# Performance work log

Hardware: AMD Instinct MI355X
Metric: run time of the kernel (lower is better)

## Reference

```python
import jax, jax.numpy as jnp
import numpy as np

N_NODES = 20000
N_EDGES = 320000
C = 64  # classes
NEG_SLOPE = 0.2  # DGL GATConv default


def setup_inputs() -> dict:
    key = jax.random.key(0)
    ks = jax.random.split(key, 32)
    dims = [C, 2 * C, 4 * C, 8 * C, 16 * C]
    inp = {}
    inp["feat"] = jax.random.normal(ks[0], (N_NODES, C), jnp.float32)
    k = 1
    for i in range(4):
        din, dout = dims[i], dims[i + 1]
        scale = 1.0 / np.sqrt(din)
        inp[f"W{i+1}"] = jax.random.normal(ks[k], (din, dout), jnp.float32) * scale; k += 1
        inp[f"al{i+1}"] = jax.random.normal(ks[k], (dout,), jnp.float32) * 0.1; k += 1
        inp[f"ar{i+1}"] = jax.random.normal(ks[k], (dout,), jnp.float32) * 0.1; k += 1
        inp[f"b{i+1}"] = jnp.zeros((dout,), jnp.float32)
    inp["relW"] = jax.random.normal(ks[k], (16 * C, C), jnp.float32) * (1.0 / np.sqrt(16 * C)); k += 1
    inp["relB"] = jnp.zeros((C,), jnp.float32)
    inp["src"] = jax.random.randint(ks[k], (N_EDGES,), 0, N_NODES, jnp.int32); k += 1
    inp["dst"] = jax.random.randint(ks[k], (N_EDGES,), 0, N_NODES, jnp.int32); k += 1
    inp["rel"] = jnp.ones((C,), jnp.int32)
    inp["order"] = 1023
    return inp


def _gat_layer(x, W, al, ar, b, src, dst, n_nodes):
    """DGL GATConv (num_heads=1, allow_zero_in_degree=True, activation=tanh)."""
    h = x @ W                                   # [N, D] projected features
    el = h @ al                                 # [N] attn_l score per node
    er = h @ ar                                 # [N] attn_r score per node
    e = jax.nn.leaky_relu(el[src] + er[dst], NEG_SLOPE)          # [E]
    # segment (edge) softmax over incoming edges of each dst node
    m = jax.ops.segment_max(e, dst, num_segments=n_nodes)        # [N]
    ex = jnp.exp(e - m[dst])                                      # [E]
    s = jax.ops.segment_sum(ex, dst, num_segments=n_nodes)       # [N]
    alpha = ex / s[dst]                                           # [E]
    # gather neighbor messages, weight by attention, scatter-add to dst
    out = jax.ops.segment_sum(h[src] * alpha[:, None], dst, num_segments=n_nodes)  # [N, D]
    return jnp.tanh(out + b)


def reference(feat, W1, al1, ar1, b1, W2, al2, ar2, b2, W3, al3, ar3, b3,
              W4, al4, ar4, b4, relW, relB, src, dst, rel, order):
    n = feat.shape[0]
    h = _gat_layer(feat, W1, al1, ar1, b1, src, dst, n)
    h = _gat_layer(h, W2, al2, ar2, b2, src, dst, n)
    h = _gat_layer(h, W3, al3, ar3, b3, src, dst, n)
    h = _gat_layer(h, W4, al4, ar4, b4, src, dst, n)
    embeddings = h[: order + 1]                  # first order+1 node embeddings
    pooling = jnp.mean(embeddings, axis=0)       # [16C]
    logits = pooling @ relW + relB               # [C]
    nz = jnp.nonzero(rel, size=rel.shape[0])[0]  # static-size nonzero (rel is all-ones)
    return logits[nz]
```

## Files before the change

kernel.cpp:

```cpp
#include <hip/hip_runtime.h>
#include <hip/hip_bf16.h>

#define NN 20000
#define NE 320000
#define MPAD 20096
#define ORD 1024

typedef __hip_bfloat16 bf16;
typedef __attribute__((ext_vector_type(8))) short bf16x8;
typedef __attribute__((ext_vector_type(4))) float f32x4;

static __device__ __forceinline__ float b2f(bf16 x) { return __bfloat162float(x); }
static __device__ __forceinline__ float bfbits2f(short s) {
    unsigned int u = ((unsigned int)(unsigned short)s) << 16;
    float f; __builtin_memcpy(&f, &u, 4); return f;
}
static __device__ __forceinline__ short f2bfbits(float v) {
    bf16 h = __float2bfloat16(v);
    short s; __builtin_memcpy(&s, &h, 2); return s;
}
static __device__ __forceinline__ unsigned short f2bfu(float v) {
    bf16 h = __float2bfloat16(v);
    unsigned short s; __builtin_memcpy(&s, &h, 2); return s;
}

__global__ void setup_all(const float* __restrict__ feat,
                          const float* __restrict__ W1, const float* __restrict__ al1, const float* __restrict__ ar1,
                          const float* __restrict__ W2, const float* __restrict__ al2, const float* __restrict__ ar2,
                          const float* __restrict__ W3, const float* __restrict__ al3, const float* __restrict__ ar3,
                          const float* __restrict__ W4, const float* __restrict__ al4, const float* __restrict__ ar4,
                          bf16* __restrict__ featb, bf16* __restrict__ wt1,
                          bf16* __restrict__ wt2, bf16* __restrict__ wt3,
                          bf16* __restrict__ wt4, int* __restrict__ counts,
                          float* __restrict__ walbuf, float* __restrict__ warbuf) {
    int b = blockIdx.x;
    if (b < 960) {
        const float *W, *al, *ar; int dout, k; float *wal, *war;
        if (b < 64)       { W = W1; al = al1; ar = ar1; dout = 128;  k = b;       wal = walbuf;        war = warbuf; }
        else if (b < 192) { W = W2; al = al2; ar = ar2; dout = 256;  k = b - 64;  wal = walbuf + 512;  war = warbuf + 512; }
        else if (b < 448) { W = W3; al = al3; ar = ar3; dout = 512;  k = b - 192; wal = walbuf + 1024; war = warbuf + 1024; }
        else              { W = W4; al = al4; ar = ar4; dout = 1024; k = b - 448; wal = walbuf + 1536; war = warbuf + 1536; }
        const float* row = W + (long)k * dout;
        float sl = 0.f, sr = 0.f;
        for (int j = threadIdx.x; j < dout; j += 256) {
            float w = row[j];
            sl += w * al[j];
            sr += w * ar[j];
        }
        __shared__ float sbl[256], sbr[256];
        sbl[threadIdx.x] = sl; sbr[threadIdx.x] = sr;
        __syncthreads();
        for (int st = 128; st > 0; st >>= 1) {
            if (threadIdx.x < st) {
                sbl[threadIdx.x] += sbl[threadIdx.x + st];
                sbr[threadIdx.x] += sbr[threadIdx.x + st];
            }
            __syncthreads();
        }
        if (threadIdx.x == 0) { wal[k] = sbl[0]; war[k] = sbr[0]; }
        return;
    }
    int i = (b - 960) * 256 + threadIdx.x;
    if (i < NN) counts[i] = 0;
    if (i < 1280000) { featb[i] = __float2bfloat16(feat[i]); return; }
    i -= 1280000;
    if (i < 8192)  { int r = i >> 7,  c = i & 127;  wt1[c * 64 + r]  = __float2bfloat16(W1[i]); return; }
    i -= 8192;
    if (i < 32768) { int r = i >> 8,  c = i & 255;  wt2[c * 128 + r] = __float2bfloat16(W2[i]); return; }
    i -= 32768;
    if (i < 131072){ int r = i >> 9,  c = i & 511;  wt3[c * 256 + r] = __float2bfloat16(W3[i]); return; }
    i -= 131072;
    if (i < 524288){ int r = i >> 10, c = i & 1023; wt4[c * 512 + r] = __float2bfloat16(W4[i]); return; }
}

__global__ void hist_kernel(const int* __restrict__ dst, int* __restrict__ counts, int n) {
    int i = blockIdx.x * blockDim.x + threadIdx.x;
    if (i < n) atomicAdd(&counts[dst[i]], 1);
}

__global__ void scan_sort(const int* __restrict__ counts, int* __restrict__ offsets,
                          int* __restrict__ cursor, int* __restrict__ nodeperm, int n) {
    const int T = 1024;
    int tid = threadIdx.x;
    int per = (n + T - 1) / T;
    int base = tid * per;
    int local = 0;
    for (int i = 0; i < per; i++) {
        int idx = base + i;
        if (idx < n) local += counts[idx];
    }
    __shared__ int sums[T];
    sums[tid] = local;
    __syncthreads();
    for (int s = 1; s < T; s <<= 1) {
        int v = (tid >= s) ? sums[tid - s] : 0;
        __syncthreads();
        sums[tid] += v;
        __syncthreads();
    }
    int run = sums[tid] - local;
    for (int i = 0; i < per; i++) {
        int idx = base + i;
        if (idx < n) {
            offsets[idx] = run;
            cursor[idx] = run;
            run += counts[idx];
        }
    }
    if (tid == T - 1) offsets[n] = run;
    __shared__ int h[256];
    __shared__ int cur[256];
    if (tid < 256) h[tid] = 0;
    __syncthreads();
    for (int i = tid; i < n; i += T) {
        int d = counts[i]; if (d > 255) d = 255;
        atomicAdd(&h[d], 1);
    }
    __syncthreads();
    int v0 = (tid < 256) ? h[tid] : 0;
    __syncthreads();
    for (int st = 1; st < 256; st <<= 1) {
        int u = (tid >= st && tid < 256) ? h[tid - st] : 0;
        __syncthreads();
        if (tid < 256) h[tid] += u;
        __syncthreads();
    }
    if (tid < 256) cur[tid] = h[tid] - v0;
    __syncthreads();
    for (int i = tid; i < n; i += T) {
        int d = counts[i]; if (d > 255) d = 255;
        int p = atomicAdd(&cur[d], 1);
        nodeperm[p] = i;
    }
}

__global__ void scatter_elr(const int* __restrict__ src, const int* __restrict__ dst,
                            int* __restrict__ cursor, int* __restrict__ esrc,
                            const bf16* __restrict__ X, const float* __restrict__ wal,
                            const float* __restrict__ war, float* __restrict__ el,
                            float* __restrict__ er) {
    int b = blockIdx.x;
    if (b < 1250) {
        int i = b * 256 + threadIdx.x;
        int p = atomicAdd(&cursor[dst[i]], 1);
        esrc[p] = src[i];
        return;
    }
    int idx = (b - 1250) * 256 + threadIdx.x;
    int node = idx >> 6;
    int lane = threadIdx.x & 63;
    if (node >= NN) return;
    float x = bfbits2f(*((const short*)X + (long)node * 64 + lane));
    float sl = x * wal[lane];
    float sr = x * war[lane];
    #pragma unroll
    for (int o = 32; o > 0; o >>= 1) {
        sl += __shfl_down(sl, o);
        sr += __shfl_down(sr, o);
    }
    if (lane == 0) { el[node] = sl; er[node] = sr; }
}

__global__ void edge_softmax_w(const int* __restrict__ off, const int* __restrict__ esrc,
                               const float* __restrict__ el, const float* __restrict__ er,
                               float* __restrict__ alpha, int n) {
    int node = blockIdx.x * 4 + (threadIdx.x >> 6);
    if (node >= n) return;
    int lane = threadIdx.x & 63;
    int s = off[node], e = off[node + 1];
    int deg = e - s;
    if (deg <= 0) return;
    float erd = er[node];
    if (deg <= 64) {
        float v = -1e30f;
        if (lane < deg) {
            float t = el[esrc[s + lane]] + erd;
            v = t >= 0.f ? t : 0.2f * t;
        }
        float mx = v;
        #pragma unroll
        for (int o = 32; o > 0; o >>= 1) mx = fmaxf(mx, __shfl_xor(mx, o));
        float x = (lane < deg) ? __expf(v - mx) : 0.f;
        float ssum = x;
        #pragma unroll
        for (int o = 32; o > 0; o >>= 1) ssum += __shfl_xor(ssum, o);
        if (lane < deg) alpha[s + lane] = x / ssum;
    } else if (deg <= 256) {
        float v[4];
        float mx = -1e30f;
        #pragma unroll
        for (int r = 0; r < 4; r++) {
            v[r] = -1e30f;
            if (r * 64 + lane < deg) {
                float t = el[esrc[s + r * 64 + lane]] + erd;
                v[r] = t >= 0.f ? t : 0.2f * t;
            }
            mx = fmaxf(mx, v[r]);
        }
        #pragma unroll
        for (int o = 32; o > 0; o >>= 1) mx = fmaxf(mx, __shfl_xor(mx, o));
        float ssum = 0.f;
        #pragma unroll
        for (int r = 0; r < 4; r++) {
            v[r] = (r * 64 + lane < deg) ? __expf(v[r] - mx) : 0.f;
            ssum += v[r];
        }
        #pragma unroll
        for (int o = 32; o > 0; o >>= 1) ssum += __shfl_xor(ssum, o);
        float inv = 1.f / ssum;
        #pragma unroll
        for (int r = 0; r < 4; r++)
            if (r * 64 + lane < deg) alpha[s + r * 64 + lane] = v[r] * inv;
    } else if (lane == 0) {
        float mx = -1e30f;
        for (int j = s; j < e; j++) {
            float t = el[esrc[j]] + erd;
            t = t >= 0.f ? t : 0.2f * t;
            alpha[j] = t;
            mx = fmaxf(mx, t);
        }
        float ssum = 0.f;
        for (int j = s; j < e; j++) { float x = __expf(alpha[j] - mx); alpha[j] = x; ssum += x; }
        float inv = 1.f / ssum;
        for (int j = s; j < e; j++) alpha[j] *= inv;
    }
}

__global__ void aggregate_e(const bf16* __restrict__ X, const float* __restrict__ alpha,
                            const int* __restrict__ esrc, const int* __restrict__ off,
                            const int* __restrict__ perm, float* __restrict__ zbuf, int zn,
                            bf16* __restrict__ Y, int din, int log2chunks, int nmax) {
    {
        int z = blockIdx.x * 256 + threadIdx.x;
        if (z < zn) zbuf[z] = 0.f;
    }
    int chunk = blockIdx.x & ((1 << log2chunks) - 1);
    int nb = blockIdx.x >> log2chunks;
    int sub = threadIdx.x >> 3, sl = threadIdx.x & 7;
    int slot = nb * 32 + sub;
    if (slot >= nmax) return;
    int node = perm ? perm[slot] : slot;
    const short* xb = (const short*)X + chunk * 64 + sl * 8;
    float acc[8] = {0.f,0.f,0.f,0.f,0.f,0.f,0.f,0.f};
    int s = off[node], e = off[node + 1];
    int j = s;
    for (; j + 8 <= e; j += 8) {
        float a[8]; int r[8]; bf16x8 w[8];
        #pragma unroll
        for (int q = 0; q < 8; q++) { a[q] = alpha[j + q]; r[q] = esrc[j + q]; }
        #pragma unroll
        for (int q = 0; q < 8; q++) w[q] = *(const bf16x8*)(xb + (long)r[q] * din);
        #pragma unroll
        for (int q = 0; q < 8; q++)
            #pragma unroll
            for (int v = 0; v < 8; v++) acc[v] += a[q] * bfbits2f(w[q][v]);
    }
    for (; j + 4 <= e; j += 4) {
        float a0 = alpha[j],     a1 = alpha[j + 1];
        float a2 = alpha[j + 2], a3 = alpha[j + 3];
        int r0 = esrc[j],     r1 = esrc[j + 1];
        int r2 = esrc[j + 2], r3 = esrc[j + 3];
        bf16x8 w0 = *(const bf16x8*)(xb + (long)r0 * din);
        bf16x8 w1 = *(const bf16x8*)(xb + (long)r1 * din);
        bf16x8 w2 = *(const bf16x8*)(xb + (long)r2 * din);
        bf16x8 w3 = *(const bf16x8*)(xb + (long)r3 * din);
        #pragma unroll
        for (int v = 0; v < 8; v++) acc[v] += a0 * bfbits2f(w0[v]);
        #pragma unroll
        for (int v = 0; v < 8; v++) acc[v] += a1 * bfbits2f(w1[v]);
        #pragma unroll
        for (int v = 0; v < 8; v++) acc[v] += a2 * bfbits2f(w2[v]);
        #pragma unroll
        for (int v = 0; v < 8; v++) acc[v] += a3 * bfbits2f(w3[v]);
    }
    for (; j < e; j++) {
        float a = alpha[j];
        bf16x8 w = *(const bf16x8*)(xb + (long)esrc[j] * din);
        #pragma unroll
        for (int v = 0; v < 8; v++) acc[v] += a * bfbits2f(w[v]);
    }
    short outv[8];
    #pragma unroll
    for (int v = 0; v < 8; v++) outv[v] = f2bfbits(acc[v]);
    bf16x8 store;
    __builtin_memcpy(&store, outv, sizeof(store));
    *(bf16x8*)((short*)Y + (long)node * din + chunk * 64 + sl * 8) = store;
}

__global__ __launch_bounds__(256, 4)
void gemm_tiled(const bf16* __restrict__ A, const bf16* __restrict__ WT,
                const float* __restrict__ bias, bf16* __restrict__ C,
                const float* __restrict__ wal, const float* __restrict__ war,
                float* __restrict__ elp, float* __restrict__ erp,
                int M, int K, int N, int ncols, int nrows) {
    __shared__ short smem[16384];
    short* As = smem;
    short* Bs = smem + 8192;
    int g = blockIdx.x;
    int rowTile = ((g >> 3) / ncols) * 8 + (g & 7);
    int colTile = (g >> 3) % ncols;
    if (rowTile >= nrows) return;
    int row0 = rowTile << 7, col0 = colTile << 7;
    int tid = threadIdx.x;
    int lane = tid & 63, wave = tid >> 6;
    int wr = (wave >> 1) << 6;
    int wc = (wave & 1) << 6;
    int m = lane & 15, quad = lane >> 4;

    f32x4 acc[4][4];
    #pragma unroll
    for (int i = 0; i < 4; i++)
        #pragma unroll
        for (int j = 0; j < 4; j++) acc[i][j] = (f32x4){0.f, 0.f, 0.f, 0.f};

    const short* Ab = (const short*)A;
    const short* Bb = (const short*)WT;
    long ga[4], gb[4];
    #pragma unroll
    for (int n = 0; n < 4; n++) {
        int chunk = n * 256 + tid;
        int row = chunk >> 3;
        int qg = (chunk & 7) ^ (row & 7);
        ga[n] = (long)(row0 + row) * K + qg * 8;
        gb[n] = (long)(col0 + row) * K + qg * 8;
    }

    typedef const __attribute__((address_space(1))) void cgvoid;
    typedef __attribute__((address_space(3))) void lvoid;

    for (int k0 = 0; k0 < K; k0 += 64) {
        __syncthreads();
        #pragma unroll
        for (int n = 0; n < 4; n++)
            __builtin_amdgcn_global_load_lds((cgvoid*)(Ab + ga[n] + k0),
                                             (lvoid*)(As + (n * 256 + tid) * 8), 16, 0, 0);
        #pragma unroll
        for (int n = 0; n < 4; n++)
            __builtin_amdgcn_global_load_lds((cgvoid*)(Bb + gb[n] + k0),
                                             (lvoid*)(Bs + (n * 256 + tid) * 8), 16, 0, 0);
        __syncthreads();
        #pragma unroll
        for (int h = 0; h < 2; h++) {
            bf16x8 af[4], bfr[4];
            #pragma unroll
            for (int s = 0; s < 4; s++) {
                int ra = wr + s * 16 + m;
                int sa = (h * 4 + quad) ^ (ra & 7);
                af[s] = *(const bf16x8*)(As + ra * 64 + sa * 8);
                int rb = wc + s * 16 + m;
                int sb = (h * 4 + quad) ^ (rb & 7);
                bfr[s] = *(const bf16x8*)(Bs + rb * 64 + sb * 8);
            }
            #pragma unroll
            for (int i = 0; i < 4; i++)
                #pragma unroll
                for (int j = 0; j < 4; j++)
                    acc[i][j] = __builtin_amdgcn_mfma_f32_16x16x32_bf16(af[i], bfr[j], acc[i][j], 0, 0, 0);
        }
    }

    float bb[4], walr[4], warr[4];
    #pragma unroll
    for (int j = 0; j < 4; j++) {
        int col = col0 + wc + j * 16 + m;
        bb[j] = bias[col];
        if (elp) { walr[j] = wal[col]; warr[j] = war[col]; }
    }
    __syncthreads();
    short* myep = smem + wave * 1152;
    #pragma unroll
    for (int i = 0; i < 4; i++) {
        float sl4[4] = {0.f, 0.f, 0.f, 0.f};
        float sr4[4] = {0.f, 0.f, 0.f, 0.f};
        #pragma unroll
        for (int j = 0; j < 4; j++) {
            #pragma unroll
            for (int r = 0; r < 4; r++) {
                float v = tanhf(acc[i][j][r] + bb[j]);
                if (elp) { sl4[r] += v * walr[j]; sr4[r] += v * warr[j]; }
                float vn = __shfl_xor(v, 1);
                if ((m & 1) == 0) {
                    unsigned int pk = (unsigned int)f2bfu(v) | ((unsigned int)f2bfu(vn) << 16);
                    *(unsigned int*)(myep + (quad * 4 + r) * 72 + j * 16 + m) = pk;
                }
            }
        }
        #pragma unroll
        for (int pass = 0; pass < 2; pass++) {
            int lr = pass * 8 + (lane >> 3);
            int lc = (lane & 7) * 8;
            bf16x8 v = *(const bf16x8*)(myep + lr * 72 + lc);
            int row = row0 + wr + i * 16 + lr;
            if (row < M)
                *(bf16x8*)((short*)C + (long)row * N + col0 + wc + lc) = v;
        }
        if (elp) {
            #pragma unroll
            for (int r = 0; r < 4; r++) {
                float s1 = sl4[r], s2 = sr4[r];
                #pragma unroll
                for (int o = 1; o < 16; o <<= 1) {
                    s1 += __shfl_xor(s1, o);
                    s2 += __shfl_xor(s2, o);
                }
                if (m == 0) {
                    int row = row0 + wr + i * 16 + quad * 4 + r;
                    if (row < M) {
                        atomicAdd(&elp[row], s1);
                        atomicAdd(&erp[row], s2);
                    }
                }
            }
        }
    }
}

__global__ void pool_sum(const bf16* __restrict__ X, const int* __restrict__ order,
                         float* __restrict__ poolsum) {
    int cg = blockIdx.x & 3, rs = blockIdx.x >> 2;
    int c = cg * 256 + threadIdx.x;
    int rows = order[0] + 1;
    float s = 0.f;
    for (int r = rs; r < rows; r += 64) s += b2f(X[(long)r * 1024 + c]);
    atomicAdd(&poolsum[c], s);
}

__global__ void head_logits(const float* __restrict__ poolsum, const float* __restrict__ relW,
                            const float* __restrict__ relB, const int* __restrict__ order,
                            float* __restrict__ logits) {
    int t = blockIdx.x;
    float s = 0.f;
    for (int c = threadIdx.x; c < 1024; c += 256)
        s += poolsum[c] * relW[(long)c * 64 + t];
    __shared__ float sb[256];
    sb[threadIdx.x] = s;
    __syncthreads();
    for (int st = 128; st > 0; st >>= 1) {
        if (threadIdx.x < st) sb[threadIdx.x] += sb[threadIdx.x + st];
        __syncthreads();
    }
    if (threadIdx.x == 0) {
        float rows = (float)(order[0] + 1);
        logits[t] = sb[0] / rows + relB[t];
    }
}

__global__ void head_gather(const float* __restrict__ logits, const int* __restrict__ rel,
                            float* __restrict__ out) {
    __shared__ int nzv[64];
    int t = threadIdx.x;
    if (t == 0) {
        int k = 0;
        for (int i = 0; i < 64; i++)
            if (rel[i] != 0) nzv[k++] = i;
        for (; k < 64; k++) nzv[k] = 0;
    }
    __syncthreads();
    out[t] = logits[nzv[t]];
}

extern "C" void kernel_launch(void* const* d_in, const int* in_sizes, int n_in,
                              void* d_out, int out_size, void* d_ws, size_t ws_size,
                              hipStream_t stream) {
    const float* feat = (const float*)d_in[0];
    const float* W[4]  = {(const float*)d_in[1], (const float*)d_in[5], (const float*)d_in[9],  (const float*)d_in[13]};
    const float* al[4] = {(const float*)d_in[2], (const float*)d_in[6], (const float*)d_in[10], (const float*)d_in[14]};
    const float* ar[4] = {(const float*)d_in[3], (const float*)d_in[7], (const float*)d_in[11], (const float*)d_in[15]};
    const float* bias[4] = {(const float*)d_in[4], (const float*)d_in[8], (const float*)d_in[12], (const float*)d_in[16]};
    const float* relW = (const float*)d_in[17];
    const float* relB = (const float*)d_in[18];
    const int* src = (const int*)d_in[19];
    const int* dst = (const int*)d_in[20];
    const int* rel = (const int*)d_in[21];
    const int* order = (const int*)d_in[22];

    const int dims[5] = {64, 128, 256, 512, 1024};

    char* p = (char*)d_ws;
    auto carve = [&](size_t bytes) {
        void* r = (void*)p;
        p += (bytes + 255) & ~(size_t)255;
        return r;
    };
    bf16* xbuf = (bf16*)carve((size_t)MPAD * 1024 * sizeof(bf16));
    bf16* ybuf = (bf16*)carve((size_t)MPAD * 512 * sizeof(bf16));
    bf16* featb = (bf16*)carve((size_t)MPAD * 64 * sizeof(bf16));
    bf16* wt[4];
    for (int l = 0; l < 4; l++)
        wt[l] = (bf16*)carve((size_t)dims[l] * dims[l + 1] * sizeof(bf16));
    float* walbuf = (float*)carve(4 * 512 * sizeof(float));
    float* warbuf = (float*)carve(4 * 512 * sizeof(float));
    float* elbuf[2];
    elbuf[0] = (float*)carve((size_t)2 * NN * sizeof(float));
    elbuf[1] = (float*)carve((size_t)2 * NN * sizeof(float));
    float* alpha = (float*)carve((size_t)NE * sizeof(float));
    int* counts  = (int*)carve((size_t)NN * sizeof(int));
    int* offsets = (int*)carve((size_t)(NN + 1) * sizeof(int));
    int* cursor  = (int*)carve((size_t)NN * sizeof(int));
    int* esrc    = (int*)carve((size_t)NE * sizeof(int));
    int* nodeperm = (int*)carve((size_t)NN * sizeof(int));
    float* poolsum = (float*)carve(1024 * sizeof(float));
    float* logits  = (float*)carve(64 * sizeof(float));

    setup_all<<<960 + 7720, 256, 0, stream>>>(
        feat, W[0], al[0], ar[0], W[1], al[1], ar[1],
        W[2], al[2], ar[2], W[3], al[3], ar[3],
        featb, wt[0], wt[1], wt[2], wt[3], counts, walbuf, warbuf);

    hist_kernel<<<(NE + 255) / 256, 256, 0, stream>>>(dst, counts, NE);
    scan_sort<<<1, 1024, 0, stream>>>(counts, offsets, cursor, nodeperm, NN);
    scatter_elr<<<1250 + 5000, 256, 0, stream>>>(src, dst, cursor, esrc,
                                                 featb, walbuf, warbuf,
                                                 elbuf[0], elbuf[0] + NN);

    const bf16* x = featb;
    const int nrows = MPAD / 128;
    const int nrowsPad = 160;
    const int log2c[4] = {0, 1, 2, 3};
    for (int l = 0; l < 4; l++) {
        int K = dims[l], N = dims[l + 1];
        float* elr_rd = elbuf[l & 1];
        float* elr_wr = elbuf[(l + 1) & 1];
        int nsm   = (l < 3) ? NN : ORD;
        int nmax  = (l < 3) ? NN : ORD;
        int nodeBlocks = (nmax + 31) / 32;
        const int* aggPerm = (l < 3) ? nodeperm : nullptr;
        edge_softmax_w<<<(nsm + 3) / 4, 256, 0, stream>>>(offsets, esrc, elr_rd,
                                                          elr_rd + NN, alpha, nsm);
        float* zbuf = (l < 3) ? elr_wr : poolsum;
        int zn = (l < 3) ? 2 * NN : 1024;
        aggregate_e<<<nodeBlocks << log2c[l], 256, 0, stream>>>(
            x, alpha, esrc, offsets, aggPerm, zbuf, zn, ybuf, K, log2c[l], nmax);
        int ncols = N >> 7;
        if (l < 3) {
            gemm_tiled<<<nrowsPad * ncols, 256, 0, stream>>>(
                ybuf, wt[l], bias[l], xbuf,
                walbuf + (l + 1) * 512, warbuf + (l + 1) * 512,
                elr_wr, elr_wr + NN,
                NN, K, N, ncols, nrows);
        } else {
            gemm_tiled<<<8 * ncols, 256, 0, stream>>>(
                ybuf, wt[l], bias[l], xbuf,
                nullptr, nullptr, nullptr, nullptr,
                ORD, K, N, ncols, 8);
        }
        x = xbuf;
    }

    pool_sum<<<256, 256, 0, stream>>>(xbuf, order, poolsum);
    head_logits<<<64, 256, 0, stream>>>(poolsum, relW, relB, order, logits);
    head_gather<<<1, 64, 0, stream>>>(logits, rel, (float*)d_out);
}
```

Measured before the change: 350.9 us.

## Parallelize CSR scan and degree sort across multiple blocks

Replaces the single-block scan_sort kernel with a two-phase multi-block scan. Phase one computes per-block sums and a global degree histogram; phase two does block-local prefix sums plus the histogram scan. The node permutation scatter moves into the existing scatter_elr launch. This removes a serial single-workgroup bottleneck at the cost of one extra launch and global atomics on the histogram cursors, which also makes the node order nondeterministic within each degree bucket.

```diff
diff --git a/kernel.cpp b/kernel.cpp
--- a/kernel.cpp
+++ b/kernel.cpp
@@ -5,6 +5,7 @@
 #define NE 320000
 #define MPAD 20096
 #define ORD 1024
+#define NB 79
 
 typedef __hip_bfloat16 bf16;
 typedef __attribute__((ext_vector_type(8))) short bf16x8;
@@ -32,6 +33,7 @@
                           bf16* __restrict__ featb, bf16* __restrict__ wt1,
                           bf16* __restrict__ wt2, bf16* __restrict__ wt3,
                           bf16* __restrict__ wt4, int* __restrict__ counts,
+                          int* __restrict__ hglob,
                           float* __restrict__ walbuf, float* __restrict__ warbuf) {
     int b = blockIdx.x;
     if (b < 960) {
@@ -62,6 +64,7 @@
     }
     int i = (b - 960) * 256 + threadIdx.x;
     if (i < NN) counts[i] = 0;
+    if (i < 256) hglob[i] = 0;
     if (i < 1280000) { featb[i] = __float2bfloat16(feat[i]); return; }
     i -= 1280000;
     if (i < 8192)  { int r = i >> 7,  c = i & 127;  wt1[c * 64 + r]  = __float2bfloat16(W1[i]); return; }
@@ -78,64 +81,77 @@
     if (i < n) atomicAdd(&counts[dst[i]], 1);
 }
 
-__global__ void scan_sort(const int* __restrict__ counts, int* __restrict__ offsets,
-                          int* __restrict__ cursor, int* __restrict__ nodeperm, int n) {
-    const int T = 1024;
+__global__ void csr_phase1(const int* __restrict__ counts, int* __restrict__ blocksums,
+                           int* __restrict__ hglob) {
+    __shared__ int sb[256];
+    __shared__ int hh[256];
     int tid = threadIdx.x;
-    int per = (n + T - 1) / T;
-    int base = tid * per;
-    int local = 0;
-    for (int i = 0; i < per; i++) {
-        int idx = base + i;
-        if (idx < n) local += counts[idx];
-    }
-    __shared__ int sums[T];
-    sums[tid] = local;
-    __syncthreads();
-    for (int s = 1; s < T; s <<= 1) {
-        int v = (tid >= s) ? sums[tid - s] : 0;
-        __syncthreads();
-        sums[tid] += v;
-        __syncthreads();
-    }
-    int run = sums[tid] - local;
-    for (int i = 0; i < per; i++) {
-        int idx = base + i;
-        if (idx < n) {
-            offsets[idx] = run;
-            cursor[idx] = run;
-            run += counts[idx];
-        }
-    }
-    if (tid == T - 1) offsets[n] = run;
-    __shared__ int h[256];
-    __shared__ int cur[256];
-    if (tid < 256) h[tid] = 0;
-    __syncthreads();
-    for (int i = tid; i < n; i += T) {
-        int d = counts[i]; if (d > 255) d = 255;
-        atomicAdd(&h[d], 1);
-    }
-    __syncthreads();
-    int v0 = (tid < 256) ? h[tid] : 0;
+    hh[tid] = 0;
+    int i = blockIdx.x * 256 + tid;
+    int c = (i < NN) ? counts[i] : 0;
+    sb[tid] = c;
+    __syncthreads();
+    for (int st = 128; st > 0; st >>= 1) {
+        if (tid < st) sb[tid] += sb[tid + st];
+        __syncthreads();
+    }
+    if (tid == 0) blocksums[blockIdx.x] = sb[0];
+    if (i < NN) {
+        int d = c > 255 ? 255 : c;
+        atomicAdd(&hh[d], 1);
+    }
+    __syncthreads();
+    if (hh[tid] > 0) atomicAdd(&hglob[tid], hh[tid]);
+}
+
+__global__ void csr_phase2(const int* __restrict__ counts, const int* __restrict__ blocksums,
+                           int* __restrict__ offsets, int* __restrict__ cursor,
+                           const int* __restrict__ hglob, int* __restrict__ curg) {
+    int tid = threadIdx.x;
+    if (blockIdx.x == NB) {
+        __shared__ int hs[256];
+        int orig = hglob[tid];
+        hs[tid] = orig;
+        __syncthreads();
+        for (int st = 1; st < 256; st <<= 1) {
+            int u = (tid >= st) ? hs[tid - st] : 0;
+            __syncthreads();
+            hs[tid] += u;
+            __syncthreads();
+        }
+        curg[tid] = hs[tid] - orig;
+        return;
+    }
+    __shared__ int bs[256];
+    bs[tid] = (tid < NB) ? blocksums[tid] : 0;
     __syncthreads();
     for (int st = 1; st < 256; st <<= 1) {
-        int u = (tid >= st && tid < 256) ? h[tid - st] : 0;
-        __syncthreads();
-        if (tid < 256) h[tid] += u;
-        __syncthreads();
-    }
-    if (tid < 256) cur[tid] = h[tid] - v0;
-    __syncthreads();
-    for (int i = tid; i < n; i += T) {
-        int d = counts[i]; if (d > 255) d = 255;
-        int p = atomicAdd(&cur[d], 1);
-        nodeperm[p] = i;
-    }
+        int u = (tid >= st) ? bs[tid - st] : 0;
+        __syncthreads();
+        bs[tid] += u;
+        __syncthreads();
+    }
+    int base = (blockIdx.x == 0) ? 0 : bs[blockIdx.x - 1];
+    __shared__ int sc[256];
+    int i = blockIdx.x * 256 + tid;
+    int c = (i < NN) ? counts[i] : 0;
+    sc[tid] = c;
+    __syncthreads();
+    for (int st = 1; st < 256; st <<= 1) {
+        int u = (tid >= st) ? sc[tid - st] : 0;
+        __syncthreads();
+        sc[tid] += u;
+        __syncthreads();
+    }
+    int excl = base + sc[tid] - c;
+    if (i < NN) { offsets[i] = excl; cursor[i] = excl; }
+    if (i == NN - 1) offsets[NN] = excl + c;
 }
 
 __global__ void scatter_elr(const int* __restrict__ src, const int* __restrict__ dst,
                             int* __restrict__ cursor, int* __restrict__ esrc,
+                            const int* __restrict__ counts, int* __restrict__ curg,
+                            int* __restrict__ nodeperm,
                             const bf16* __restrict__ X, const float* __restrict__ wal,
                             const float* __restrict__ war, float* __restrict__ el,
                             float* __restrict__ er) {
@@ -146,7 +162,16 @@
         esrc[p] = src[i];
         return;
     }
-    int idx = (b - 1250) * 256 + threadIdx.x;
+    if (b < 1250 + NB) {
+        int i = (b - 1250) * 256 + threadIdx.x;
+        if (i < NN) {
+            int d = counts[i]; if (d > 255) d = 255;
+            int p = atomicAdd(&curg[d], 1);
+            nodeperm[p] = i;
+        }
+        return;
+    }
+    int idx = (b - 1250 - NB) * 256 + threadIdx.x;
     int node = idx >> 6;
     int lane = threadIdx.x & 63;
     if (node >= NN) return;
@@ -499,19 +524,24 @@
     int* cursor  = (int*)carve((size_t)NN * sizeof(int));
     int* esrc    = (int*)carve((size_t)NE * sizeof(int));
     int* nodeperm = (int*)carve((size_t)NN * sizeof(int));
+    int* blocksums = (int*)carve((size_t)NB * sizeof(int));
+    int* hglob   = (int*)carve(256 * sizeof(int));
+    int* curg    = (int*)carve(256 * sizeof(int));
     float* poolsum = (float*)carve(1024 * sizeof(float));
     float* logits  = (float*)carve(64 * sizeof(float));
 
     setup_all<<<960 + 7720, 256, 0, stream>>>(
         feat, W[0], al[0], ar[0], W[1], al[1], ar[1],
         W[2], al[2], ar[2], W[3], al[3], ar[3],
-        featb, wt[0], wt[1], wt[2], wt[3], counts, walbuf, warbuf);
+        featb, wt[0], wt[1], wt[2], wt[3], counts, hglob, walbuf, warbuf);
 
     hist_kernel<<<(NE + 255) / 256, 256, 0, stream>>>(dst, counts, NE);
-    scan_sort<<<1, 1024, 0, stream>>>(counts, offsets, cursor, nodeperm, NN);
-    scatter_elr<<<1250 + 5000, 256, 0, stream>>>(src, dst, cursor, esrc,
-                                                 featb, walbuf, warbuf,
-                                                 elbuf[0], elbuf[0] + NN);
+    csr_phase1<<<NB, 256, 0, stream>>>(counts, blocksums, hglob);
+    csr_phase2<<<NB + 1, 256, 0, stream>>>(counts, blocksums, offsets, cursor, hglob, curg);
+    scatter_elr<<<1250 + NB + 5000, 256, 0, stream>>>(src, dst, cursor, esrc,
+                                                      counts, curg, nodeperm,
+                                                      featb, walbuf, warbuf,
+                                                      elbuf[0], elbuf[0] + NN);
 
     const bf16* x = featb;
     const int nrows = MPAD / 128;
```

Measured after the change: 359.3 us. 1.02x slower.
